# Kernel tuning notes

Hardware: AMD Instinct MI355X
Metric: run time of the kernel (lower is better)

The kernel has to match this reference:

```python
import jax, jax.numpy as jnp
import numpy as np

C = 64
RED = 4            # attention reduction: conv_match C -> C//RED
CR = C // RED      # 16, also MultiScaleSpatialAttention reduced channels
N_HASHES = 4
CHUNK = 512
RES_SCALE = 0.1
EPS = 5e-5


def conv2d(x, w, b=None, padding=0, groups=1):
    out = jax.lax.conv_general_dilated(
        x, w, (1, 1), [(padding, padding), (padding, padding)],
        dimension_numbers=('NCHW', 'OIHW', 'NCHW'), feature_group_count=groups)
    if b is not None:
        out = out + b[None, :, None, None]
    return out


def ds_conv(x, pw_w, dw_w, dw_b, padding):
    # pointwise (no bias) then depthwise (bias)
    x = conv2d(x, pw_w)
    return conv2d(x, dw_w, dw_b, padding=padding, groups=dw_w.shape[0])


def pool2(x, mode):
    B, Cc, H, W = x.shape
    xr = x.reshape(B, Cc, H // 2, 2, W // 2, 2)
    return xr.max(axis=(3, 5)) if mode == 'max' else xr.mean(axis=(3, 5))


def bilinear_ac(x, out_h, out_w):
    # bilinear interpolation with align_corners=True (matches F.interpolate)
    B, Cc, h, w = x.shape
    def coords(n_in, n_out):
        pos = jnp.arange(n_out, dtype=x.dtype) * ((n_in - 1) / (n_out - 1))
        lo = jnp.floor(pos).astype(jnp.int32)
        hi = jnp.minimum(lo + 1, n_in - 1)
        frac = pos - lo.astype(x.dtype)
        return lo, hi, frac
    lo_h, hi_h, fh = coords(h, out_h)
    x = x[:, :, lo_h, :] * (1 - fh)[None, None, :, None] + x[:, :, hi_h, :] * fh[None, None, :, None]
    lo_w, hi_w, fw = coords(w, out_w)
    x = x[:, :, :, lo_w] * (1 - fw) + x[:, :, :, hi_w] * fw
    return x


def sparse_attn(x, wm, bm, wa, ba, rot):
    # NLSN-style LSH-chunked non-local sparse attention
    N, Cc, H, W = x.shape
    L = H * W
    xe = conv2d(x, wm, bm).reshape(N, -1, L).transpose(0, 2, 1)   # [N,L,Ce]
    ye = conv2d(x, wa, ba).reshape(N, -1, L).transpose(0, 2, 1)   # [N,L,C]
    Ce = xe.shape[-1]
    n_chunks = L // CHUNK                     # L multiple of CHUNK here -> no padding
    buckets = min(n_chunks + n_chunks % 2, 128)
    # LSH hashing (rot: [Ce, n_hashes, buckets//2])
    rv = jnp.einsum('blf,fhi->bhli', xe, rot)
    rv = jnp.concatenate([rv, -rv], axis=-1)  # [N,nh,L,buckets]
    codes = jnp.argmax(rv, axis=-1) + (jnp.arange(N_HASHES) * buckets)[None, :, None]
    codes = codes.reshape(N, -1)              # [N, nh*L]
    idx = jnp.argsort(codes, axis=-1)
    undo = jnp.argsort(idx, axis=-1)
    mod_idx = idx % L
    xs = jnp.take_along_axis(xe, mod_idx[:, :, None], axis=1)     # [N,nh*L,Ce]
    ys = jnp.take_along_axis(ye, mod_idx[:, :, None], axis=1)     # [N,nh*L,C]
    xb = xs.reshape(N, N_HASHES, n_chunks, CHUNK, Ce)
    yb = ys.reshape(N, N_HASHES, n_chunks, CHUNK, Cc)
    xm = xb / jnp.maximum(jnp.linalg.norm(xb, axis=-1, keepdims=True), EPS)
    def adj(t):  # add previous / next bucket (circular)
        return jnp.concatenate([t, jnp.roll(t, 1, axis=2), jnp.roll(t, -1, axis=2)], axis=3)
    xm3, yb3 = adj(xm), adj(yb)
    raw = jnp.einsum('bhkie,bhkje->bhkij', xb, xm3)               # [N,nh,k,CHUNK,3*CHUNK]
    bscore = jax.nn.logsumexp(raw, axis=-1, keepdims=True)
    score = jnp.exp(raw - bscore)
    ret = jnp.einsum('bhkij,bhkje->bhkie', score, yb3)            # [N,nh,k,CHUNK,C]
    ret = ret.reshape(N, N_HASHES * L, Cc)
    bscore = bscore.reshape(N, N_HASHES * L)
    ret = jnp.take_along_axis(ret, undo[:, :, None], axis=1).reshape(N, N_HASHES, L, Cc)
    bscore = jnp.take_along_axis(bscore, undo, axis=1).reshape(N, N_HASHES, L, 1)
    probs = jax.nn.softmax(bscore, axis=1)                        # over hash rounds
    out = (ret * probs).sum(axis=1)                               # [N,L,C]
    out = out.transpose(0, 2, 1).reshape(N, Cc, H, W)
    return out * RES_SCALE + x


def setup_inputs() -> dict:
    key = jax.random.key(0)
    ks = iter(jax.random.split(key, 40))
    w = lambda *s: jax.random.normal(next(ks), s, jnp.float32) * 0.1
    inp = {
        'x': jax.random.normal(next(ks), (2, C, 128, 128), jnp.float32),
        'spa_down_w': w(CR, C, 1, 1), 'spa_down_b': w(CR),
        's0_pw_w': w(2 * CR, CR, 1, 1), 's0_dw_w': w(2 * CR, 1, 1, 1), 's0_dw_b': w(2 * CR),
        'br3_pw_w': w(CR, CR, 1, 1), 'br3_dw_w': w(CR, 1, 3, 3), 'br3_dw_b': w(CR),
        'br5_pw_w': w(CR, CR, 1, 1), 'br5_dw_w': w(CR, 1, 5, 5), 'br5_dw_b': w(CR),
        'br7_pw_w': w(CR, CR, 1, 1), 'br7_dw_w': w(CR, 1, 7, 7), 'br7_dw_b': w(CR),
        'fusion_w': w(C, 8 * CR, 1, 1), 'fusion_b': w(C),
        'resid_w': w(C, C, 1, 1), 'resid_b': w(C),
        'ca_w1': w(C // 16, C, 1, 1), 'ca_b1': w(C // 16),
        'ca_w2': w(C, C // 16, 1, 1), 'ca_b2': w(C),
        'conv1x1_w': w(C, C, 1, 1), 'conv1x1_b': w(C),
        'match_w': w(CR, C, 1, 1), 'match_b': w(CR),
        'asm_w': w(C, C, 1, 1), 'asm_b': w(C),
        'rot': jax.random.normal(next(ks), (CR, N_HASHES, 16), jnp.float32),  # buckets//2 = 16
        'collect_w': w(C, C, 1, 1), 'collect_b': w(C),
    }
    return inp


def reference(x, spa_down_w, spa_down_b, s0_pw_w, s0_dw_w, s0_dw_b,
              br3_pw_w, br3_dw_w, br3_dw_b, br5_pw_w, br5_dw_w, br5_dw_b,
              br7_pw_w, br7_dw_w, br7_dw_b, fusion_w, fusion_b,
              resid_w, resid_b, ca_w1, ca_b1, ca_w2, ca_b2,
              conv1x1_w, conv1x1_b, match_w, match_b, asm_w, asm_b, rot,
              collect_w, collect_b):
    B, Cc, H, W = x.shape
    # --- MultiScaleSpatialAttention ---
    xr = conv2d(x, spa_down_w, spa_down_b)                # [B,16,H,W]
    s0 = ds_conv(xr, s0_pw_w, s0_dw_w, s0_dw_b, padding=0)
    feats = [s0]
    for pw, dw, db, pad in ((br3_pw_w, br3_dw_w, br3_dw_b, 1),
                            (br5_pw_w, br5_dw_w, br5_dw_b, 2),
                            (br7_pw_w, br7_dw_w, br7_dw_b, 3)):
        mx = ds_conv(pool2(xr, 'max'), pw, dw, db, pad)
        av = ds_conv(pool2(xr, 'avg'), pw, dw, db, pad)
        feats.append(jnp.concatenate([bilinear_ac(mx, H, W), bilinear_ac(av, H, W)], axis=1))
    attn = jax.nn.sigmoid(conv2d(jnp.concatenate(feats, axis=1), fusion_w, fusion_b))
    spa_mask = x * attn + conv2d(x, resid_w, resid_b)
    # --- CALayer ---
    y = x.mean(axis=(2, 3), keepdims=True)
    y = jax.nn.sigmoid(conv2d(jax.nn.relu(conv2d(y, ca_w1, ca_b1)), ca_w2, ca_b2))
    spe_mask = x * y
    # --- combine + SparseMaskConv (n_layers=1: attention then 1x1 collect) ---
    mask = conv2d(spa_mask + spe_mask, conv1x1_w, conv1x1_b) + x
    fea = sparse_attn(mask, match_w, match_b, asm_w, asm_b, rot)
    out1 = conv2d(fea, collect_w, collect_b)
    return out1 + x
```

## Files before the change

kernel.cpp:

```cpp
#include <hip/hip_runtime.h>
#include <math.h>

static constexpr int NB = 2;
static constexpr int NC = 64;
static constexpr int NHp = 128, NWp = 128;
static constexpr int NL = NHp * NWp;
static constexpr int NCR = 16;
static constexpr int NL2 = 64 * 64;
static constexpr int NHASH = 4;
static constexpr int CHUNKSZ = 512;
static constexpr int NCHUNKS = 32;
static constexpr int TOT = NHASH * NL;
static constexpr int NKEY = 128;
static constexpr int NTILE = 256;
static constexpr int TILESZ = TOT / NTILE;

typedef _Float16 half4 __attribute__((ext_vector_type(4)));
typedef _Float16 half8 __attribute__((ext_vector_type(8)));
typedef float f32x4 __attribute__((ext_vector_type(4)));

static constexpr size_t OFF_MASK = 0;
static constexpr size_t OFF_FEA  = OFF_MASK + (size_t)NB*NC*NL;
static constexpr size_t OFF_XE   = OFF_FEA  + (size_t)NB*NC*NL;
static constexpr size_t OFF_XEH  = OFF_XE   + (size_t)NB*NL*NCR;
static constexpr size_t OFF_XENH = OFF_XEH  + (size_t)NB*NL*NCR/2;
static constexpr size_t OFF_YEH  = OFF_XENH + (size_t)NB*NL*NCR/2;
static constexpr size_t OFF_RET  = OFF_YEH  + (size_t)NB*NL*NC/2;
static constexpr size_t OFF_BSC  = OFF_RET  + (size_t)NB*TOT*NC/2;
static constexpr size_t OFF_INT  = OFF_BSC  + (size_t)NB*TOT;
static constexpr size_t IOFF_CODES = 0;
static constexpr size_t IOFF_IDX   = IOFF_CODES + (size_t)NB*TOT;
static constexpr size_t IOFF_UNDO  = IOFF_IDX   + (size_t)NB*TOT;
static constexpr size_t IOFF_HIST  = IOFF_UNDO  + (size_t)NB*TOT;
static constexpr size_t IOFF_OFFS  = IOFF_HIST  + (size_t)NB*NKEY*NTILE/2;
static constexpr size_t IOFF_END   = IOFF_OFFS  + (size_t)NB*NKEY*NTILE/2;
static constexpr size_t OFF_CAY = OFF_INT + IOFF_END;
static constexpr size_t OFF_CAS = OFF_CAY + 128;
static constexpr size_t OFF_CRW = OFF_CAS + 128;
static constexpr size_t OFF_CRB = OFF_CRW + 4096;
static constexpr size_t OFF_PMX   = OFF_FEA;
static constexpr size_t OFF_PAV   = OFF_PMX  + (size_t)NB*NCR*NL2;
static constexpr size_t OFF_PTMP  = OFF_PAV  + (size_t)NB*NCR*NL2;
static constexpr size_t OFF_DWT   = OFF_PTMP + (size_t)6*NB*NCR*NL2;
static_assert(OFF_DWT + (size_t)6*NB*NCR*NL2 <= OFF_XE, "halfres overlay fits");
static constexpr size_t OFF_XR    = OFF_XE;
static constexpr size_t OFF_FEATS = OFF_XR + (size_t)NB*NCR*NL;
static_assert(OFF_FEATS + (size_t)NB*128*NL <= OFF_BSC, "feats overlay fits");
static constexpr size_t OFF_PRE1  = OFF_FEA;

__device__ __forceinline__ float sigmoidf_(float v){ return 1.0f/(1.0f + expf(-v)); }


__global__ __launch_bounds__(256,4) void k_xr(const float* __restrict__ x,
                     const float* __restrict__ w,
                     const float* __restrict__ b, float* __restrict__ xr){
  int gid = blockIdx.x*256 + threadIdx.x;
  int pix = gid >> 1, hf = gid & 1;
  int bb = pix >> 14, p = pix & (NL-1);
  const float* xi = x + (size_t)bb*NC*NL + (size_t)hf*32*NL + p;
  float acc[16];
  #pragma unroll
  for (int oc=0; oc<16; ++oc) acc[oc] = hf ? 0.f : b[oc];
  for (int ic0=0; ic0<32; ic0+=16){
    float r[16];
    #pragma unroll
    for (int j=0; j<16; ++j) r[j] = xi[(size_t)(ic0+j)*NL];
    #pragma unroll
    for (int oc=0; oc<16; ++oc){
      #pragma unroll
      for (int j=0; j<16; ++j) acc[oc] += r[j]*w[oc*64 + hf*32 + ic0 + j];
    }
  }
  #pragma unroll
  for (int oc=0; oc<16; ++oc) acc[oc] += __shfl_xor(acc[oc], 1, 64);
  if (!hf){
    float* xo = xr + (size_t)bb*NCR*NL + p;
    #pragma unroll
    for (int oc=0; oc<16; ++oc) xo[(size_t)oc*NL] = acc[oc];
  }
}

__global__ __launch_bounds__(256,4) void k_s0(const float* __restrict__ xr,
                     const float* __restrict__ pw,
                     const float* __restrict__ dww, const float* __restrict__ dwb,
                     float* __restrict__ feats){
  int gid = blockIdx.x*256 + threadIdx.x;
  int oc0 = blockIdx.y*16;
  int bb = gid >> 14, p = gid & (NL-1);
  const float* xi = xr + (size_t)bb*NCR*NL + p;
  float r[16];
  #pragma unroll
  for (int ic=0; ic<16; ++ic) r[ic] = xi[(size_t)ic*NL];
  float* fo = feats + (size_t)bb*128*NL + p;
  #pragma unroll
  for (int j=0; j<16; ++j){
    int oc = oc0 + j;
    float s = 0.f;
    #pragma unroll
    for (int ic=0; ic<16; ++ic) s += r[ic]*pw[oc*16+ic];
    fo[(size_t)oc*NL] = s*dww[oc] + dwb[oc];
  }
}

__global__ void k_pool(const float* __restrict__ xr, float* __restrict__ pmax,
                       float* __restrict__ pavg){
  int gid = blockIdx.x*256 + threadIdx.x;
  if (gid >= NB*NCR*NL2) return;
  int p = gid & (NL2-1); int t = gid >> 12; int c = t & 15; int bb = t >> 4;
  int y = p >> 6, x2 = p & 63;
  const float* base = xr + (size_t)(bb*NCR + c)*NL + (size_t)(2*y)*NWp + 2*x2;
  float a = base[0], b_ = base[1], c_ = base[NWp], d = base[NWp+1];
  pmax[gid] = fmaxf(fmaxf(a,b_), fmaxf(c_,d));
  pavg[gid] = 0.25f*(a+b_+c_+d);
}

__global__ void k_pw16_all(const float* __restrict__ pmx, const float* __restrict__ pav,
                           const float* __restrict__ w0, const float* __restrict__ w1,
                           const float* __restrict__ w2, float* __restrict__ out){
  int gid = blockIdx.x*256 + threadIdx.x;
  if (gid >= 6*NB*NL2) return;
  int p = gid & (NL2-1); int t = gid >> 12; int bb = t & 1; int combo = t >> 1;
  int br = combo >> 1, mode = combo & 1;
  const float* w = (br==0) ? w0 : (br==1) ? w1 : w2;
  const float* in = ((mode==0) ? pmx : pav) + (size_t)bb*NCR*NL2 + p;
  float r[16];
  #pragma unroll
  for (int ic=0; ic<16; ++ic) r[ic] = in[(size_t)ic*NL2];
  float* oo = out + ((size_t)(combo*NB + bb)*NCR)*NL2 + p;
  #pragma unroll
  for (int oc=0; oc<16; ++oc){
    float s = 0.f;
    #pragma unroll
    for (int ic=0; ic<16; ++ic) s += r[ic]*w[oc*16+ic];
    oo[(size_t)oc*NL2] = s;
  }
}

__global__ void k_dw_all(const float* __restrict__ in,
                         const float* __restrict__ w3, const float* __restrict__ b3,
                         const float* __restrict__ w5, const float* __restrict__ b5,
                         const float* __restrict__ w7, const float* __restrict__ b7,
                         float* __restrict__ out){
  int gid = blockIdx.x*256 + threadIdx.x;
  if (gid >= 6*NB*NCR*NL2) return;
  int p = gid & (NL2-1); int t = gid >> 12; int c = t & 15; int r2 = t >> 4;
  int bb = r2 & 1; int combo = r2 >> 1;
  int br = combo >> 1;
  int K = (br==0) ? 3 : (br==1) ? 5 : 7; int P = K >> 1;
  const float* w = (br==0) ? w3 : (br==1) ? w5 : w7;
  const float* bias = (br==0) ? b3 : (br==1) ? b5 : b7;
  int y = p >> 6, x = p & 63;
  const float* xi = in + ((size_t)(combo*NB + bb)*NCR + c)*NL2;
  float s = bias[c];
  for (int dy=0; dy<K; ++dy){
    int iy = y + dy - P;
    if ((unsigned)iy < 64u){
      for (int dx=0; dx<K; ++dx){
        int ix = x + dx - P;
        if ((unsigned)ix < 64u) s += xi[iy*64 + ix] * w[(c*K + dy)*K + dx];
      }
    }
  }
  out[gid] = s;
}

__global__ void k_up_all(const float* __restrict__ in, float* __restrict__ feats){
  int gid = blockIdx.x*256 + threadIdx.x;
  if (gid >= 6*NB*NCR*NL) return;
  int p = gid & (NL-1); int t = gid >> 14; int c = t & 15; int r2 = t >> 4;
  int bb = r2 & 1; int combo = r2 >> 1;
  int y = p >> 7, x = p & 127;
  const float sc = 63.0f/127.0f;
  float fy = y*sc; int ly = (int)floorf(fy); int hy = min(ly+1, 63); fy -= (float)ly;
  float fx = x*sc; int lx = (int)floorf(fx); int hx = min(lx+1, 63); float gx = fx - (float)lx;
  const float* xi = in + ((size_t)(combo*NB + bb)*NCR + c)*NL2;
  float v0 = xi[ly*64+lx]*(1.f-fy) + xi[hy*64+lx]*fy;
  float v1 = xi[ly*64+hx]*(1.f-fy) + xi[hy*64+hx]*fy;
  int coff = 32 + combo*16 + c;
  feats[(size_t)bb*128*NL + (size_t)coff*NL + p] = v0*(1.f-gx) + v1*gx;
}

__global__ void k_camean(const float* __restrict__ x, float* __restrict__ cay){
  __shared__ float red[256];
  int bc = blockIdx.x; int tid = threadIdx.x;
  float s = 0.f;
  for (int i = tid; i < NL; i += 256) s += x[(size_t)bc*NL + i];
  red[tid] = s; __syncthreads();
  for (int st=128; st>0; st>>=1){ if (tid<st) red[tid]+=red[tid+st]; __syncthreads(); }
  if (tid==0) cay[bc] = red[0] / (float)NL;
}

__global__ void k_camlp(const float* __restrict__ cay,
                        const float* __restrict__ w1, const float* __restrict__ b1,
                        const float* __restrict__ w2, const float* __restrict__ b2,
                        float* __restrict__ cas){
  __shared__ float z[NB*4];
  int tid = threadIdx.x;
  if (tid < NB*4){
    int bb = tid >> 2, j = tid & 3;
    float s = b1[j];
    for (int ic=0; ic<NC; ++ic) s += cay[bb*NC+ic]*w1[j*NC+ic];
    z[tid] = fmaxf(s, 0.f);
  }
  __syncthreads();
  if (tid < NB*NC){
    int bb = tid >> 6, oc = tid & 63;
    float s = b2[oc];
    #pragma unroll
    for (int j=0; j<4; ++j) s += z[bb*4+j]*w2[oc*4+j];
    cas[tid] = sigmoidf_(s);
  }
}

__global__ void k_wprod(const float* __restrict__ c11w, const float* __restrict__ c11b,
                        const float* __restrict__ rw, const float* __restrict__ rb,
                        float* __restrict__ crw, float* __restrict__ crb){
  int gid = blockIdx.x*256 + threadIdx.x;
  if (gid >= 4096) return;
  int o = gid >> 6, i = gid & 63;
  float s = 0.f;
  for (int k=0; k<64; ++k) s += c11w[o*64+k]*rw[k*64+i];
  crw[gid] = s;
  if (i == 0){
    float t = c11b[o];
    for (int k=0; k<64; ++k) t += c11w[o*64+k]*rb[k];
    crb[o] = t;
  }
}

__global__ __launch_bounds__(256,4) void k_attnmul(const float* __restrict__ x,
                          const float* __restrict__ feats,
                          const float* __restrict__ fw, const float* __restrict__ fb,
                          const float* __restrict__ cas, float* __restrict__ pre1){
  int gid = blockIdx.x*256 + threadIdx.x;
  int oc0 = blockIdx.y*16;
  int bb = gid >> 14, p = gid & (NL-1);
  const float* fi = feats + (size_t)bb*128*NL + p;
  float acc[16];
  #pragma unroll
  for (int j=0; j<16; ++j) acc[j] = fb[oc0+j];
  for (int k0=0; k0<128; k0+=8){
    float fr[8];
    #pragma unroll
    for (int j=0; j<8; ++j) fr[j] = fi[(size_t)(k0+j)*NL];
    #pragma unroll
    for (int j=0; j<16; ++j){
      #pragma unroll
      for (int t=0; t<8; ++t) acc[j] += fr[t]*fw[(oc0+j)*128+k0+t];
    }
  }
  const float* xb = x + (size_t)bb*NC*NL + p;
  float* po = pre1 + (size_t)bb*NC*NL + p;
  #pragma unroll
  for (int j=0; j<16; ++j){
    int oc = oc0 + j;
    float xv = xb[(size_t)oc*NL];
    po[(size_t)oc*NL] = xv*(sigmoidf_(acc[j]) + cas[bb*64+oc]);
  }
}

__global__ __launch_bounds__(256,4) void k_mask(const float* __restrict__ pre1,
                       const float* __restrict__ c11w,
                       const float* __restrict__ crw, const float* __restrict__ crb,
                       const float* __restrict__ x, float* __restrict__ mask){
  int gid = blockIdx.x*256 + threadIdx.x;
  int oc0 = blockIdx.y*16;
  int bb = gid >> 14, p = gid & (NL-1);
  const float* pi = pre1 + (size_t)bb*NC*NL + p;
  const float* xi = x + (size_t)bb*NC*NL + p;
  float acc[16];
  #pragma unroll
  for (int j=0; j<16; ++j) acc[j] = crb[oc0+j];
  for (int ic0=0; ic0<64; ic0+=8){
    float pr[8], xr8[8];
    #pragma unroll
    for (int j=0; j<8; ++j){ pr[j] = pi[(size_t)(ic0+j)*NL]; xr8[j] = xi[(size_t)(ic0+j)*NL]; }
    #pragma unroll
    for (int j=0; j<16; ++j){
      #pragma unroll
      for (int t=0; t<8; ++t)
        acc[j] += pr[t]*c11w[(oc0+j)*64+ic0+t] + xr8[t]*crw[(oc0+j)*64+ic0+t];
    }
  }
  float* mo = mask + (size_t)bb*NC*NL + p;
  #pragma unroll
  for (int j=0; j<16; ++j){
    int oc = oc0 + j;
    mo[(size_t)oc*NL] = acc[j] + xi[(size_t)oc*NL];
  }
}


__global__ __launch_bounds__(256,4) void k_xe(const float* __restrict__ mask,
                     const float* __restrict__ w, const float* __restrict__ b,
                     const float* __restrict__ rot,
                     _Float16* __restrict__ xeh, _Float16* __restrict__ xenh,
                     int* __restrict__ codes, int* __restrict__ hist){
  int gid = blockIdx.x*256 + threadIdx.x;
  int pix = gid >> 1, hf = gid & 1;
  int bb = pix >> 14, l = pix & (NL-1);
  const float* mi = mask + (size_t)bb*NC*NL + (size_t)hf*32*NL + l;
  float acc[16];
  #pragma unroll
  for (int oc=0; oc<16; ++oc) acc[oc] = hf ? 0.f : b[oc];
  for (int ic0=0; ic0<32; ic0+=16){
    float r[16];
    #pragma unroll
    for (int j=0; j<16; ++j) r[j] = mi[(size_t)(ic0+j)*NL];
    #pragma unroll
    for (int oc=0; oc<16; ++oc){
      #pragma unroll
      for (int j=0; j<16; ++j) acc[oc] += r[j]*w[oc*64 + hf*32 + ic0 + j];
    }
  }
  #pragma unroll
  for (int oc=0; oc<16; ++oc) acc[oc] += __shfl_xor(acc[oc], 1, 64);
  if (!hf){
    float n2 = 0.f;
    #pragma unroll
    for (int oc=0; oc<16; ++oc) n2 += acc[oc]*acc[oc];
    float inv = 1.0f / fmaxf(sqrtf(n2), 5e-5f);
    _Float16* ho = xeh + (size_t)pix*NCR;
    _Float16* no = xenh + (size_t)pix*NCR;
    #pragma unroll
    for (int g=0; g<4; ++g){
      half4 hv, nv;
      #pragma unroll
      for (int j=0; j<4; ++j){ hv[j] = (_Float16)acc[g*4+j]; nv[j] = (_Float16)(acc[g*4+j]*inv); }
      *(half4*)(ho + g*4) = hv;
      *(half4*)(no + g*4) = nv;
    }
  }
  #pragma unroll
  for (int hh=0; hh<2; ++hh){
    int h = hf*2 + hh;
    float rv[16];
    #pragma unroll
    for (int i=0; i<16; ++i){
      float s = 0.f;
      #pragma unroll
      for (int f=0; f<16; ++f) s += acc[f]*rot[(f*NHASH + h)*16 + i];
      rv[i] = s;
    }
    float best = -1e30f; int bi = 0;
    #pragma unroll
    for (int i=0; i<16; ++i){ if (rv[i] > best){ best = rv[i]; bi = i; } }
    #pragma unroll
    for (int i=0; i<16; ++i){ float val = -rv[i]; if (val > best){ best = val; bi = 16+i; } }
    int code = bi + h*32;
    codes[((bb*NHASH + h) << 14) + l] = code;
    int tile = h*64 + (l >> 8);
    atomicAdd(&hist[bb*NKEY*NTILE + code*NTILE + tile], 1);
  }
}

__global__ __launch_bounds__(256,4) void k_yeh(const float* __restrict__ mask,
                      const float* __restrict__ w,
                      const float* __restrict__ b, _Float16* __restrict__ yeh){
  int gid = blockIdx.x*256 + threadIdx.x;
  int oc0 = blockIdx.y*16;
  int bb = gid >> 14, l = gid & (NL-1);
  const float* mi = mask + (size_t)bb*NC*NL + l;
  float acc[16];
  #pragma unroll
  for (int j=0; j<16; ++j) acc[j] = b[oc0+j];
  for (int ic0=0; ic0<64; ic0+=8){
    float r[8];
    #pragma unroll
    for (int j=0; j<8; ++j) r[j] = mi[(size_t)(ic0+j)*NL];
    #pragma unroll
    for (int j=0; j<16; ++j){
      #pragma unroll
      for (int t=0; t<8; ++t) acc[j] += r[t]*w[(oc0+j)*64+ic0+t];
    }
  }
  _Float16* yo = yeh + (size_t)(bb*NL + l)*NC + oc0;
  #pragma unroll
  for (int g=0; g<2; ++g){
    half8 h;
    #pragma unroll
    for (int j=0; j<8; ++j) h[j] = (_Float16)acc[g*8+j];
    *(half8*)(yo + g*8) = h;
  }
}

__global__ void k_scan(const int* __restrict__ hist, int* __restrict__ offs){
  __shared__ int part[256];
  int bb = blockIdx.x; int t = threadIdx.x;
  const int* hi = hist + (size_t)bb*NKEY*NTILE;
  int* oo = offs + (size_t)bb*NKEY*NTILE;
  int s = 0;
  for (int i=0; i<128; ++i) s += hi[t*128 + i];
  part[t] = s; __syncthreads();
  int v = s;
  for (int off=1; off<256; off<<=1){
    int u = (t >= off) ? part[t-off] : 0;
    __syncthreads();
    v += u; part[t] = v;
    __syncthreads();
  }
  int run = v - s;
  for (int i=0; i<128; ++i){ int q = hi[t*128+i]; oo[t*128+i] = run; run += q; }
}

__global__ __launch_bounds__(256) void k_scatter(const int* __restrict__ codes,
                          const int* __restrict__ offs,
                          int* __restrict__ idx, int* __restrict__ undo){
  __shared__ int cnt[4][NKEY];
  int wid = threadIdx.x >> 6, lane = threadIdx.x & 63;
  int t4 = blockIdx.x;
  int bb = t4 >> 6;
  int tile = (t4 & 63)*4 + wid;
  cnt[wid][lane] = 0; cnt[wid][64+lane] = 0;
  const int* cb = codes + bb*TOT;
  const int* ob = offs + (size_t)bb*NKEY*NTILE;
  int* ib = idx + bb*TOT;
  int* ub = undo + bb*TOT;
  for (int g=0; g<4; ++g){
    int j = tile*TILESZ + g*64 + lane;
    int k = cb[j];
    unsigned long long m = ~0ull;
    #pragma unroll
    for (int bit=0; bit<7; ++bit){
      unsigned long long bmask = __ballot((k >> bit) & 1);
      m &= ((k >> bit) & 1) ? bmask : ~bmask;
    }
    int rank = __popcll(m & ((1ull << lane) - 1ull));
    int leader = __ffsll((unsigned long long)m) - 1;
    int base = 0;
    if (lane == leader){
      base = cnt[wid][k];
      cnt[wid][k] = base + __popcll(m);
    }
    base = __shfl(base, leader, 64);
    int pos = ob[k*NTILE + tile] + base + rank;
    ib[pos] = j;
    ub[j] = pos;
    __threadfence_block();
  }
}

__global__ __launch_bounds__(512) void k_attn(
    const _Float16* __restrict__ xeh, const _Float16* __restrict__ xenh,
    const _Float16* __restrict__ yeh, const int* __restrict__ idx,
    _Float16* __restrict__ retb, float* __restrict__ bsc){
  __shared__ _Float16 kt[64*24];
  __shared__ _Float16 vt[64*70];
  int blk = blockIdx.x;
  int qq = blk & 3; int kk = (blk >> 2) & 31; int h = (blk >> 7) & 3; int bb = blk >> 9;
  int tid = threadIdx.x;
  int w = tid >> 6, lane = tid & 63, col = lane & 15, grp = lane >> 4;
  const int* idxb = idx + bb*TOT;
  int posq = h*NL + kk*CHUNKSZ + qq*128 + w*16 + col;
  int lq = idxb[posq] & (NL-1);
  half4 qfr = *(const half4*)(xeh + ((size_t)bb*NL + lq)*16 + grp*4);

  f32x4 O[4];
  #pragma unroll
  for (int a=0; a<4; ++a) O[a] = (f32x4){0.f,0.f,0.f,0.f};
  float m_ = -1e30f, ssum = 0.f;

  for (int t=0; t<24; ++t){
    __syncthreads();
    {
      int kx = tid & 63, c0 = (tid >> 6) * 8;
      int jj = t*64 + kx; int sec = jj >> 9; int j0 = jj & 511;
      int cc = kk + ((sec==1) ? -1 : (sec==2) ? 1 : 0);
      cc = (cc + NCHUNKS) & (NCHUNKS-1);
      int lv = idxb[h*NL + cc*CHUNKSZ + j0] & (NL-1);
      half8 vv = *(const half8*)(yeh + ((size_t)bb*NL + lv)*64 + c0);
      #pragma unroll
      for (int j=0; j<8; ++j) vt[(c0+j)*70 + kx] = vv[j];
    }
    if (tid < 128){
      int r = tid >> 1, hf = tid & 1;
      int jj = t*64 + r; int sec = jj >> 9; int j0 = jj & 511;
      int cc = kk + ((sec==1) ? -1 : (sec==2) ? 1 : 0);
      cc = (cc + NCHUNKS) & (NCHUNKS-1);
      int lk = idxb[h*NL + cc*CHUNKSZ + j0] & (NL-1);
      *(half8*)(kt + r*24 + hf*8) =
          *(const half8*)(xenh + ((size_t)bb*NL + lk)*16 + hf*8);
    }
    __syncthreads();

    f32x4 S[4];
    #pragma unroll
    for (int kb=0; kb<4; ++kb){
      half4 ka = *(const half4*)(kt + (kb*16 + col)*24 + grp*4);
      S[kb] = __builtin_amdgcn_mfma_f32_16x16x16f16(
          ka, qfr, (f32x4){0.f,0.f,0.f,0.f}, 0, 0, 0);
    }

    float mtl = -1e30f;
    #pragma unroll
    for (int kb=0; kb<4; ++kb)
      #pragma unroll
      for (int i=0; i<4; ++i) mtl = fmaxf(mtl, S[kb][i]);
    if (__any(mtl > m_ + 8.0f)){
      float mt = fmaxf(mtl, __shfl_xor(mtl, 16, 64));
      mt = fmaxf(mt, __shfl_xor(mt, 32, 64));
      float mn = fmaxf(m_, mt);
      float sc = __expf(m_ - mn);
      ssum *= sc;
      m_ = mn;
      #pragma unroll
      for (int cf=0; cf<4; ++cf)
        #pragma unroll
        for (int i=0; i<4; ++i) O[cf][i] *= sc;
    }
    half4 pf[4];
    float ps = 0.f;
    #pragma unroll
    for (int kb=0; kb<4; ++kb){
      #pragma unroll
      for (int i=0; i<4; ++i){
        float p = __expf(S[kb][i] - m_);
        ps += p;
        pf[kb][i] = (_Float16)p;
      }
    }
    ssum += ps;

    #pragma unroll
    for (int cf=0; cf<4; ++cf){
      #pragma unroll
      for (int kb=0; kb<4; ++kb){
        half4 va = *(const half4*)(vt + (cf*16 + col)*70 + kb*16 + grp*4);
        O[cf] = __builtin_amdgcn_mfma_f32_16x16x16f16(
            va, pf[kb], O[cf], 0, 0, 0);
      }
    }
  }

  ssum += __shfl_xor(ssum, 16, 64);
  ssum += __shfl_xor(ssum, 32, 64);
  float inv = 1.0f/ssum;
  size_t rb = ((size_t)bb*TOT + posq)*64;
  #pragma unroll
  for (int cf=0; cf<4; ++cf){
    half4 o;
    #pragma unroll
    for (int i=0; i<4; ++i) o[i] = (_Float16)(O[cf][i]*inv);
    *(half4*)(retb + rb + cf*16 + grp*4) = o;
  }
  if (grp == 0) bsc[(size_t)bb*TOT + posq] = m_ + logf(ssum);
}

__global__ __launch_bounds__(256,4) void k_combine(const _Float16* __restrict__ retb,
                          const float* __restrict__ bsc,
                          const int* __restrict__ undo, const float* __restrict__ mask,
                          float* __restrict__ fea){
  int gid = blockIdx.x*256 + threadIdx.x;
  int c0 = blockIdx.y*32;
  int bb = gid >> 14; int l = gid & (NL-1);
  const int* ub = undo + bb*TOT;
  int pos[4]; float sc[4];
  #pragma unroll
  for (int h=0; h<4; ++h){ pos[h] = ub[h*NL + l]; sc[h] = bsc[bb*TOT + pos[h]]; }
  float mx = fmaxf(fmaxf(sc[0],sc[1]), fmaxf(sc[2],sc[3]));
  float e[4]; float tot = 0.f;
  #pragma unroll
  for (int h=0; h<4; ++h){ e[h] = __expf(sc[h]-mx); tot += e[h]; }
  float inv = 0.1f/tot;
  const float* mb_ = mask + (size_t)bb*NC*NL + l;
  float* fo = fea + (size_t)bb*NC*NL + l;
  const _Float16* r0 = retb + ((size_t)bb*TOT + pos[0])*NC + c0;
  const _Float16* r1 = retb + ((size_t)bb*TOT + pos[1])*NC + c0;
  const _Float16* r2 = retb + ((size_t)bb*TOT + pos[2])*NC + c0;
  const _Float16* r3 = retb + ((size_t)bb*TOT + pos[3])*NC + c0;
  #pragma unroll
  for (int g=0; g<4; ++g){
    half8 v0 = *(const half8*)(r0 + g*8);
    half8 v1 = *(const half8*)(r1 + g*8);
    half8 v2 = *(const half8*)(r2 + g*8);
    half8 v3 = *(const half8*)(r3 + g*8);
    #pragma unroll
    for (int j=0; j<8; ++j){
      int c = c0 + g*8 + j;
      float v = (float)v0[j]*e[0] + (float)v1[j]*e[1] + (float)v2[j]*e[2] + (float)v3[j]*e[3];
      fo[(size_t)c*NL] = v*inv + mb_[(size_t)c*NL];
    }
  }
}

__global__ __launch_bounds__(256,4) void k_collect(const float* __restrict__ fea,
                          const float* __restrict__ w,
                          const float* __restrict__ b, const float* __restrict__ x,
                          float* __restrict__ out){
  int gid = blockIdx.x*256 + threadIdx.x;
  int oc0 = blockIdx.y*16;
  int bb = gid >> 14, p = gid & (NL-1);
  const float* fi = fea + (size_t)bb*NC*NL + p;
  const float* xi = x + (size_t)bb*NC*NL + p;
  float acc[16];
  #pragma unroll
  for (int j=0; j<16; ++j) acc[j] = b[oc0+j];
  for (int ic0=0; ic0<64; ic0+=8){
    float r[8];
    #pragma unroll
    for (int j=0; j<8; ++j) r[j] = fi[(size_t)(ic0+j)*NL];
    #pragma unroll
    for (int j=0; j<16; ++j){
      #pragma unroll
      for (int t=0; t<8; ++t) acc[j] += r[t]*w[(oc0+j)*64+ic0+t];
    }
  }
  float* oo = out + (size_t)bb*NC*NL + p;
  #pragma unroll
  for (int j=0; j<16; ++j){
    int oc = oc0 + j;
    oo[(size_t)oc*NL] = acc[j] + xi[(size_t)oc*NL];
  }
}

extern "C" void kernel_launch(void* const* d_in, const int* in_sizes, int n_in,
                              void* d_out, int out_size, void* d_ws, size_t ws_size,
                              hipStream_t stream) {
  const float* x        = (const float*)d_in[0];
  const float* spa_dw   = (const float*)d_in[1];
  const float* spa_db   = (const float*)d_in[2];
  const float* s0_pw    = (const float*)d_in[3];
  const float* s0_dww   = (const float*)d_in[4];
  const float* s0_dwb   = (const float*)d_in[5];
  const float* fus_w    = (const float*)d_in[15];
  const float* fus_b    = (const float*)d_in[16];
  const float* res_w    = (const float*)d_in[17];
  const float* res_b    = (const float*)d_in[18];
  const float* ca_w1    = (const float*)d_in[19];
  const float* ca_b1    = (const float*)d_in[20];
  const float* ca_w2    = (const float*)d_in[21];
  const float* ca_b2    = (const float*)d_in[22];
  const float* c11_w    = (const float*)d_in[23];
  const float* c11_b    = (const float*)d_in[24];
  const float* match_w  = (const float*)d_in[25];
  const float* match_b  = (const float*)d_in[26];
  const float* asm_w    = (const float*)d_in[27];
  const float* asm_b    = (const float*)d_in[28];
  const float* rot      = (const float*)d_in[29];
  const float* col_w    = (const float*)d_in[30];
  const float* col_b    = (const float*)d_in[31];
  float* out = (float*)d_out;

  float* ws    = (float*)d_ws;
  float* mask  = ws + OFF_MASK;
  float* fea   = ws + OFF_FEA;
  _Float16* xeh  = (_Float16*)(ws + OFF_XEH);
  _Float16* xenh = (_Float16*)(ws + OFF_XENH);
  _Float16* yeh  = (_Float16*)(ws + OFF_YEH);
  _Float16* retb = (_Float16*)(ws + OFF_RET);
  float* bsc   = ws + OFF_BSC;
  int*   ib    = (int*)(ws + OFF_INT);
  int* codes   = ib + IOFF_CODES;
  int* idx     = ib + IOFF_IDX;
  int* undo    = ib + IOFF_UNDO;
  int* hist    = ib + IOFF_HIST;
  int* offs    = ib + IOFF_OFFS;
  float* cay   = ws + OFF_CAY;
  float* cas   = ws + OFF_CAS;
  float* crw   = ws + OFF_CRW;
  float* crb   = ws + OFF_CRB;
  float* xr    = ws + OFF_XR;
  float* feats = ws + OFF_FEATS;
  float* pmx   = ws + OFF_PMX;
  float* pav   = ws + OFF_PAV;
  float* ptmp  = ws + OFF_PTMP;
  float* dwt   = ws + OFF_DWT;
  float* pre1  = ws + OFF_PRE1;

  k_xr<<<(NB*NL*2)/256, 256, 0, stream>>>(x, spa_dw, spa_db, xr);
  k_wprod<<<16, 256, 0, stream>>>(c11_w, c11_b, res_w, res_b, crw, crb);
  k_s0<<<dim3((NB*NL)/256, 2), 256, 0, stream>>>(xr, s0_pw, s0_dww, s0_dwb, feats);
  k_pool<<<(NB*NCR*NL2)/256, 256, 0, stream>>>(xr, pmx, pav);
  k_pw16_all<<<(6*NB*NL2)/256, 256, 0, stream>>>(pmx, pav,
      (const float*)d_in[6], (const float*)d_in[9], (const float*)d_in[12], ptmp);
  k_dw_all<<<(6*NB*NCR*NL2)/256, 256, 0, stream>>>(ptmp,
      (const float*)d_in[7], (const float*)d_in[8],
      (const float*)d_in[10], (const float*)d_in[11],
      (const float*)d_in[13], (const float*)d_in[14], dwt);
  k_up_all<<<(6*NB*NCR*NL)/256, 256, 0, stream>>>(dwt, feats);
  k_camean<<<NB*NC, 256, 0, stream>>>(x, cay);
  k_camlp<<<1, 128, 0, stream>>>(cay, ca_w1, ca_b1, ca_w2, ca_b2, cas);
  k_attnmul<<<dim3((NB*NL)/256, 4), 256, 0, stream>>>(x, feats, fus_w, fus_b, cas, pre1);
  k_mask<<<dim3((NB*NL)/256, 4), 256, 0, stream>>>(pre1, c11_w, crw, crb, x, mask);

  hipMemsetAsync(hist, 0, (size_t)NB*NKEY*NTILE*sizeof(int), stream);
  k_xe<<<(NB*NL*2)/256, 256, 0, stream>>>(mask, match_w, match_b, rot, xeh, xenh, codes, hist);
  k_yeh<<<dim3((NB*NL)/256, 4), 256, 0, stream>>>(mask, asm_w, asm_b, yeh);
  k_scan<<<NB, 256, 0, stream>>>(hist, offs);
  k_scatter<<<NB*NTILE/4, 256, 0, stream>>>(codes, offs, idx, undo);
  k_attn<<<NB*NHASH*NCHUNKS*4, 512, 0, stream>>>(xeh, xenh, yeh, idx, retb, bsc);
  k_combine<<<dim3((NB*NL)/256, 2), 256, 0, stream>>>(retb, bsc, undo, mask, fea);
  k_collect<<<dim3((NB*NL)/256, 4), 256, 0, stream>>>(fea, col_w, col_b, x, out);
}
```

Baseline: 361.2 us.

## Pre-sort Q/K/V into bucket order and process two query tiles per wave

The value projection now scatters its fp16 output straight into hash-sorted order via the undo permutation, and a new gather kernel writes sorted copies of queries and keys. The attention kernel therefore reads contiguous sorted rows instead of doing indirect lookups through idx. Each wave also handles two 16-query fragments, and PV uses the 16x16x32 MFMA. Together these halve the block count and reuse each K/V tile across more queries. The cost is extra write traffic for the sorted copies (V is duplicated per hash) and higher register pressure in the attention kernel.

Result: faster. 328.6 us (-9.0%).

```diff
diff --git a/kernel.cpp b/kernel.cpp
--- a/kernel.cpp
+++ b/kernel.cpp
@@ -24,8 +24,8 @@
 static constexpr size_t OFF_XE   = OFF_FEA  + (size_t)NB*NC*NL;
 static constexpr size_t OFF_XEH  = OFF_XE   + (size_t)NB*NL*NCR;
 static constexpr size_t OFF_XENH = OFF_XEH  + (size_t)NB*NL*NCR/2;
-static constexpr size_t OFF_YEH  = OFF_XENH + (size_t)NB*NL*NCR/2;
-static constexpr size_t OFF_RET  = OFF_YEH  + (size_t)NB*NL*NC/2;
+static constexpr size_t OFF_VS   = OFF_XENH + (size_t)NB*NL*NCR/2;
+static constexpr size_t OFF_RET  = OFF_VS   + (size_t)NB*TOT*NC/2;
 static constexpr size_t OFF_BSC  = OFF_RET  + (size_t)NB*TOT*NC/2;
 static constexpr size_t OFF_INT  = OFF_BSC  + (size_t)NB*TOT;
 static constexpr size_t IOFF_CODES = 0;
@@ -38,6 +38,9 @@
 static constexpr size_t OFF_CAS = OFF_CAY + 128;
 static constexpr size_t OFF_CRW = OFF_CAS + 128;
 static constexpr size_t OFF_CRB = OFF_CRW + 4096;
+static constexpr size_t OFF_QS = OFF_FEA;
+static constexpr size_t OFF_KS = OFF_QS + (size_t)NB*TOT*NCR/2;
+static_assert(OFF_KS + (size_t)NB*TOT*NCR/2 <= OFF_XE, "qs/ks fit in fea region");
 static constexpr size_t OFF_PMX   = OFF_FEA;
 static constexpr size_t OFF_PAV   = OFF_PMX  + (size_t)NB*NCR*NL2;
 static constexpr size_t OFF_PTMP  = OFF_PAV  + (size_t)NB*NCR*NL2;
@@ -45,7 +48,7 @@
 static_assert(OFF_DWT + (size_t)6*NB*NCR*NL2 <= OFF_XE, "halfres overlay fits");
 static constexpr size_t OFF_XR    = OFF_XE;
 static constexpr size_t OFF_FEATS = OFF_XR + (size_t)NB*NCR*NL;
-static_assert(OFF_FEATS + (size_t)NB*128*NL <= OFF_BSC, "feats overlay fits");
+static_assert(OFF_FEATS + (size_t)NB*128*NL <= OFF_RET, "feats overlay fits");
 static constexpr size_t OFF_PRE1  = OFF_FEA;
 
 __device__ __forceinline__ float sigmoidf_(float v){ return 1.0f/(1.0f + expf(-v)); }
@@ -355,8 +358,8 @@
 }
 
 __global__ __launch_bounds__(256,4) void k_yeh(const float* __restrict__ mask,
-                      const float* __restrict__ w,
-                      const float* __restrict__ b, _Float16* __restrict__ yeh){
+                      const float* __restrict__ w, const float* __restrict__ b,
+                      const int* __restrict__ undo, _Float16* __restrict__ vs){
   int gid = blockIdx.x*256 + threadIdx.x;
   int oc0 = blockIdx.y*16;
   int bb = gid >> 14, l = gid & (NL-1);
@@ -374,14 +377,29 @@
       for (int t=0; t<8; ++t) acc[j] += r[t]*w[(oc0+j)*64+ic0+t];
     }
   }
-  _Float16* yo = yeh + (size_t)(bb*NL + l)*NC + oc0;
-  #pragma unroll
-  for (int g=0; g<2; ++g){
-    half8 h;
-    #pragma unroll
-    for (int j=0; j<8; ++j) h[j] = (_Float16)acc[g*8+j];
-    *(half8*)(yo + g*8) = h;
-  }
+  half8 h0, h1;
+  #pragma unroll
+  for (int j=0; j<8; ++j){ h0[j] = (_Float16)acc[j]; h1[j] = (_Float16)acc[8+j]; }
+  const int* ub = undo + bb*TOT;
+  #pragma unroll
+  for (int h=0; h<4; ++h){
+    int pos = ub[h*NL + l];
+    _Float16* vo = vs + ((size_t)bb*TOT + pos)*64 + oc0;
+    *(half8*)(vo) = h0;
+    *(half8*)(vo + 8) = h1;
+  }
+}
+
+__global__ __launch_bounds__(256,4) void k_gather(const int* __restrict__ idx,
+                      const _Float16* __restrict__ xeh, const _Float16* __restrict__ xenh,
+                      _Float16* __restrict__ qs, _Float16* __restrict__ ks){
+  int gid = blockIdx.x*256 + threadIdx.x;
+  int pos = gid >> 1, hf = gid & 1;
+  int bb = pos >> 16;
+  int p = pos & (TOT-1);
+  int l = idx[bb*TOT + p] & (NL-1);
+  *(half8*)(qs + (size_t)pos*16 + hf*8) = *(const half8*)(xeh + ((size_t)bb*NL + l)*16 + hf*8);
+  *(half8*)(ks + (size_t)pos*16 + hf*8) = *(const half8*)(xenh + ((size_t)bb*NL + l)*16 + hf*8);
 }
 
 __global__ void k_scan(const int* __restrict__ hist, int* __restrict__ offs){
@@ -441,24 +459,31 @@
 }
 
 __global__ __launch_bounds__(512) void k_attn(
-    const _Float16* __restrict__ xeh, const _Float16* __restrict__ xenh,
-    const _Float16* __restrict__ yeh, const int* __restrict__ idx,
+    const _Float16* __restrict__ qs, const _Float16* __restrict__ ks,
+    const _Float16* __restrict__ vs,
     _Float16* __restrict__ retb, float* __restrict__ bsc){
-  __shared__ _Float16 kt[64*24];
+  __shared__ _Float16 kt[64*20];
   __shared__ _Float16 vt[64*70];
   int blk = blockIdx.x;
-  int qq = blk & 3; int kk = (blk >> 2) & 31; int h = (blk >> 7) & 3; int bb = blk >> 9;
+  int qh = blk & 1; int kk = (blk >> 1) & 31; int h = (blk >> 6) & 3; int bb = blk >> 8;
   int tid = threadIdx.x;
   int w = tid >> 6, lane = tid & 63, col = lane & 15, grp = lane >> 4;
-  const int* idxb = idx + bb*TOT;
-  int posq = h*NL + kk*CHUNKSZ + qq*128 + w*16 + col;
-  int lq = idxb[posq] & (NL-1);
-  half4 qfr = *(const half4*)(xeh + ((size_t)bb*NL + lq)*16 + grp*4);
-
-  f32x4 O[4];
-  #pragma unroll
-  for (int a=0; a<4; ++a) O[a] = (f32x4){0.f,0.f,0.f,0.f};
-  float m_ = -1e30f, ssum = 0.f;
+  int qbase = h*NL + kk*CHUNKSZ + qh*256 + w*32;
+
+  half4 qfr[2]; int posq[2];
+  #pragma unroll
+  for (int qf=0; qf<2; ++qf){
+    posq[qf] = qbase + qf*16 + col;
+    qfr[qf] = *(const half4*)(qs + ((size_t)bb*TOT + posq[qf])*16 + grp*4);
+  }
+
+  f32x4 O[4][2];
+  #pragma unroll
+  for (int a=0; a<4; ++a)
+    #pragma unroll
+    for (int b=0; b<2; ++b) O[a][b] = (f32x4){0.f,0.f,0.f,0.f};
+  float m_[2] = {-1e30f,-1e30f};
+  float ssum[2] = {0.f,0.f};
 
   for (int t=0; t<24; ++t){
     __syncthreads();
@@ -467,8 +492,8 @@
       int jj = t*64 + kx; int sec = jj >> 9; int j0 = jj & 511;
       int cc = kk + ((sec==1) ? -1 : (sec==2) ? 1 : 0);
       cc = (cc + NCHUNKS) & (NCHUNKS-1);
-      int lv = idxb[h*NL + cc*CHUNKSZ + j0] & (NL-1);
-      half8 vv = *(const half8*)(yeh + ((size_t)bb*NL + lv)*64 + c0);
+      int spos = h*NL + cc*CHUNKSZ + j0;
+      half8 vv = *(const half8*)(vs + ((size_t)bb*TOT + spos)*64 + c0);
       #pragma unroll
       for (int j=0; j<8; ++j) vt[(c0+j)*70 + kx] = vv[j];
     }
@@ -477,73 +502,92 @@
       int jj = t*64 + r; int sec = jj >> 9; int j0 = jj & 511;
       int cc = kk + ((sec==1) ? -1 : (sec==2) ? 1 : 0);
       cc = (cc + NCHUNKS) & (NCHUNKS-1);
-      int lk = idxb[h*NL + cc*CHUNKSZ + j0] & (NL-1);
-      *(half8*)(kt + r*24 + hf*8) =
-          *(const half8*)(xenh + ((size_t)bb*NL + lk)*16 + hf*8);
+      int spos = h*NL + cc*CHUNKSZ + j0;
+      *(half8*)(kt + r*20 + hf*8) =
+          *(const half8*)(ks + ((size_t)bb*TOT + spos)*16 + hf*8);
     }
     __syncthreads();
 
-    f32x4 S[4];
+    f32x4 S[4][2];
     #pragma unroll
     for (int kb=0; kb<4; ++kb){
-      half4 ka = *(const half4*)(kt + (kb*16 + col)*24 + grp*4);
-      S[kb] = __builtin_amdgcn_mfma_f32_16x16x16f16(
-          ka, qfr, (f32x4){0.f,0.f,0.f,0.f}, 0, 0, 0);
-    }
-
-    float mtl = -1e30f;
-    #pragma unroll
-    for (int kb=0; kb<4; ++kb)
-      #pragma unroll
-      for (int i=0; i<4; ++i) mtl = fmaxf(mtl, S[kb][i]);
-    if (__any(mtl > m_ + 8.0f)){
-      float mt = fmaxf(mtl, __shfl_xor(mtl, 16, 64));
-      mt = fmaxf(mt, __shfl_xor(mt, 32, 64));
-      float mn = fmaxf(m_, mt);
-      float sc = __expf(m_ - mn);
-      ssum *= sc;
-      m_ = mn;
-      #pragma unroll
-      for (int cf=0; cf<4; ++cf)
+      half4 ka = *(const half4*)(kt + (kb*16 + col)*20 + grp*4);
+      #pragma unroll
+      for (int qf=0; qf<2; ++qf)
+        S[kb][qf] = __builtin_amdgcn_mfma_f32_16x16x16f16(
+            ka, qfr[qf], (f32x4){0.f,0.f,0.f,0.f}, 0, 0, 0);
+    }
+
+    half4 pf[2][4];
+    #pragma unroll
+    for (int qf=0; qf<2; ++qf){
+      float mtl = -1e30f;
+      #pragma unroll
+      for (int kb=0; kb<4; ++kb)
         #pragma unroll
-        for (int i=0; i<4; ++i) O[cf][i] *= sc;
-    }
-    half4 pf[4];
-    float ps = 0.f;
-    #pragma unroll
-    for (int kb=0; kb<4; ++kb){
-      #pragma unroll
-      for (int i=0; i<4; ++i){
-        float p = __expf(S[kb][i] - m_);
-        ps += p;
-        pf[kb][i] = (_Float16)p;
+        for (int i=0; i<4; ++i) mtl = fmaxf(mtl, S[kb][qf][i]);
+      if (__any(mtl > m_[qf] + 8.0f)){
+        float mt = fmaxf(mtl, __shfl_xor(mtl, 16, 64));
+        mt = fmaxf(mt, __shfl_xor(mt, 32, 64));
+        float mn = fmaxf(m_[qf], mt);
+        float sc = __expf(m_[qf] - mn);
+        ssum[qf] *= sc;
+        m_[qf] = mn;
+        #pragma unroll
+        for (int cf=0; cf<4; ++cf)
+          #pragma unroll
+          for (int i=0; i<4; ++i) O[cf][qf][i] *= sc;
       }
-    }
-    ssum += ps;
+      float ps = 0.f;
+      #pragma unroll
+      for (int kb=0; kb<4; ++kb){
+        #pragma unroll
+        for (int i=0; i<4; ++i){
+          float p = __expf(S[kb][qf][i] - m_[qf]);
+          ps += p;
+          pf[qf][kb][i] = (_Float16)p;
+        }
+      }
+      ssum[qf] += ps;
+    }
 
     #pragma unroll
     for (int cf=0; cf<4; ++cf){
       #pragma unroll
-      for (int kb=0; kb<4; ++kb){
-        half4 va = *(const half4*)(vt + (cf*16 + col)*70 + kb*16 + grp*4);
-        O[cf] = __builtin_amdgcn_mfma_f32_16x16x16f16(
-            va, pf[kb], O[cf], 0, 0, 0);
+      for (int k2=0; k2<2; ++k2){
+        half4 a0 = *(const half4*)(vt + (cf*16 + col)*70 + k2*32 + grp*4);
+        half4 a1 = *(const half4*)(vt + (cf*16 + col)*70 + k2*32 + 16 + grp*4);
+        half8 va;
+        #pragma unroll
+        for (int i=0; i<4; ++i){ va[i] = a0[i]; va[4+i] = a1[i]; }
+        #pragma unroll
+        for (int qf=0; qf<2; ++qf){
+          half8 pb;
+          #pragma unroll
+          for (int i=0; i<4; ++i){ pb[i] = pf[qf][2*k2][i]; pb[4+i] = pf[qf][2*k2+1][i]; }
+          O[cf][qf] = __builtin_amdgcn_mfma_f32_16x16x32_f16(
+              va, pb, O[cf][qf], 0, 0, 0);
+        }
       }
     }
   }
 
-  ssum += __shfl_xor(ssum, 16, 64);
-  ssum += __shfl_xor(ssum, 32, 64);
-  float inv = 1.0f/ssum;
-  size_t rb = ((size_t)bb*TOT + posq)*64;
-  #pragma unroll
-  for (int cf=0; cf<4; ++cf){
-    half4 o;
-    #pragma unroll
-    for (int i=0; i<4; ++i) o[i] = (_Float16)(O[cf][i]*inv);
-    *(half4*)(retb + rb + cf*16 + grp*4) = o;
-  }
-  if (grp == 0) bsc[(size_t)bb*TOT + posq] = m_ + logf(ssum);
+  #pragma unroll
+  for (int qf=0; qf<2; ++qf){
+    float st = ssum[qf];
+    st += __shfl_xor(st, 16, 64);
+    st += __shfl_xor(st, 32, 64);
+    float inv = 1.0f/st;
+    size_t rb = ((size_t)bb*TOT + posq[qf])*64;
+    #pragma unroll
+    for (int cf=0; cf<4; ++cf){
+      half4 o;
+      #pragma unroll
+      for (int i=0; i<4; ++i) o[i] = (_Float16)(O[cf][qf][i]*inv);
+      *(half4*)(retb + rb + cf*16 + grp*4) = o;
+    }
+    if (grp == 0) bsc[(size_t)bb*TOT + posq[qf]] = m_[qf] + logf(st);
+  }
 }
 
 __global__ __launch_bounds__(256,4) void k_combine(const _Float16* __restrict__ retb,
@@ -646,7 +690,9 @@
   float* fea   = ws + OFF_FEA;
   _Float16* xeh  = (_Float16*)(ws + OFF_XEH);
   _Float16* xenh = (_Float16*)(ws + OFF_XENH);
-  _Float16* yeh  = (_Float16*)(ws + OFF_YEH);
+  _Float16* vsort = (_Float16*)(ws + OFF_VS);
+  _Float16* qsort = (_Float16*)(ws + OFF_QS);
+  _Float16* ksort = (_Float16*)(ws + OFF_KS);
   _Float16* retb = (_Float16*)(ws + OFF_RET);
   float* bsc   = ws + OFF_BSC;
   int*   ib    = (int*)(ws + OFF_INT);
@@ -685,10 +731,11 @@
 
   hipMemsetAsync(hist, 0, (size_t)NB*NKEY*NTILE*sizeof(int), stream);
   k_xe<<<(NB*NL*2)/256, 256, 0, stream>>>(mask, match_w, match_b, rot, xeh, xenh, codes, hist);
-  k_yeh<<<dim3((NB*NL)/256, 4), 256, 0, stream>>>(mask, asm_w, asm_b, yeh);
   k_scan<<<NB, 256, 0, stream>>>(hist, offs);
   k_scatter<<<NB*NTILE/4, 256, 0, stream>>>(codes, offs, idx, undo);
-  k_attn<<<NB*NHASH*NCHUNKS*4, 512, 0, stream>>>(xeh, xenh, yeh, idx, retb, bsc);
+  k_yeh<<<dim3((NB*NL)/256, 4), 256, 0, stream>>>(mask, asm_w, asm_b, undo, vsort);
+  k_gather<<<(NB*TOT*2)/256, 256, 0, stream>>>(idx, xeh, xenh, qsort, ksort);
+  k_attn<<<NB*NHASH*NCHUNKS*2, 512, 0, stream>>>(qsort, ksort, vsort, retb, bsc);
   k_combine<<<dim3((NB*NL)/256, 2), 256, 0, stream>>>(retb, bsc, undo, mask, fea);
   k_collect<<<dim3((NB*NL)/256, 4), 256, 0, stream>>>(fea, col_w, col_b, x, out);
 }
```
